# Kernel tuning notes

Measured on AMD Instinct MI355X. Metric: run time of the kernel, lower is better.

## Reference

```python
import jax, jax.numpy as jnp
import numpy as np

NUM_HEADS = 12
ROPE_BASE = 10000.0


def _rope_cache(u, v, head_dim):
    # u, v: [n, L] normalized coords; P pairs per axis = head_dim // 4
    P = head_dim // 2 // 2
    freqs = jnp.arange(P) / (P - 1 + 1e-09)
    inv = 1.0 / ROPE_BASE ** freqs
    ang_x = jnp.einsum('nl,f->nlf', u, inv)
    ang_y = jnp.einsum('nl,f->nlf', v, inv)
    return jnp.cos(ang_x), jnp.sin(ang_x), jnp.cos(ang_y), jnp.sin(ang_y)


def _rope_apply(t, cos_x, sin_x, cos_y, sin_y):
    # t: [n, L, H, D]
    n, L, H, D = t.shape
    q = t.reshape(n, L, H, D // 2, 2)
    ppa = (D // 2) // 2  # pairs per axis
    qx, qy = jnp.split(q, [ppa], axis=-2)

    def rotate(qp, c, s):
        c = c[:, :, None, :]
        s = s[:, :, None, :]
        x, y = qp[..., 0], qp[..., 1]
        return jnp.stack([x * c - y * s, x * s + y * c], axis=-1)

    qx = rotate(qx, cos_x, sin_x)
    qy = rotate(qy, cos_y, sin_y)
    return jnp.concatenate([qx, qy], axis=-2).reshape(n, L, H, D)


def setup_inputs() -> dict:
    key = jax.random.key(0)
    ks = jax.random.split(key, 10)
    n, L, d = 16, 1024, 768
    H = NUM_HEADS
    D = d // H
    glorot = jax.nn.initializers.xavier_uniform()
    return {
        'inputs_q': jax.random.normal(ks[0], (n, L, d), jnp.float32),
        'inputs_kv': jax.random.normal(ks[1], (n, L, d), jnp.float32),
        'Wq': glorot(ks[2], (d, H, D), jnp.float32),
        'bq': jnp.zeros((H, D), jnp.float32),
        'Wk': glorot(ks[3], (d, H, D), jnp.float32),
        'bk': jnp.zeros((H, D), jnp.float32),
        'Wv': glorot(ks[4], (d, H, D), jnp.float32),
        'bv': jnp.zeros((H, D), jnp.float32),
        'Wo': glorot(ks[5], (H, D, d), jnp.float32),
        'bo': jnp.zeros((d,), jnp.float32),
    }


def reference(inputs_q, inputs_kv, Wq, bq, Wk, bk, Wv, bv, Wo, bo):
    n, L, d = inputs_q.shape
    H = NUM_HEADS
    D = d // H

    q = jnp.einsum('nld,dhk->nlhk', inputs_q, Wq) + bq
    k = jnp.einsum('nld,dhk->nlhk', inputs_kv, Wk) + bk
    v = jnp.einsum('nld,dhk->nlhk', inputs_kv, Wv) + bv

    # square-grid 2D RoPE coordinates (rope_uv=None fallback)
    h = w = int(np.sqrt(L))
    ys, xs = np.mgrid[:h, :w]
    u = jnp.tile(((xs.reshape(-1) + 0.5) / w).astype(np.float32)[None, :], (n, 1))
    vv = jnp.tile(((ys.reshape(-1) + 0.5) / h).astype(np.float32)[None, :], (n, 1))
    cos_x, sin_x, cos_y, sin_y = _rope_cache(u, vv, D)

    q = _rope_apply(q, cos_x, sin_x, cos_y, sin_y)
    k = _rope_apply(k, cos_x, sin_x, cos_y, sin_y)

    scale = 1.0 / jnp.sqrt(jnp.float32(D))
    attn_logits = jnp.einsum('nqhd,nkhd->nhqk', q, k) * scale
    attn = jax.nn.softmax(attn_logits, axis=-1)
    out = jnp.einsum('nhqk,nkhd->nqhd', attn, v)
    return jnp.einsum('nqhd,hdm->nqm', out, Wo) + bo
```

## Files before the change

kernel.cpp:

```cpp
#include <hip/hip_runtime.h>
#include <cmath>

#define DMODEL 768
#define SEQ    1024
#define NH     12
#define HDIM   64
#define MTOT   16384

typedef unsigned short ushort_t;
typedef __attribute__((ext_vector_type(8))) short short8v;
typedef __attribute__((ext_vector_type(4))) float f32x4;
typedef __attribute__((ext_vector_type(16))) float f32x16;
typedef __attribute__((ext_vector_type(2))) int i32x2v;

union v8u { short8v v; unsigned u[4]; };

__device__ __forceinline__ ushort_t bf16rn(float x) {
  unsigned u = __float_as_uint(x);
  return (ushort_t)((u + 0x7FFFu + ((u >> 16) & 1u)) >> 16);
}
__device__ __forceinline__ void bsplit(float x, ushort_t& h, ushort_t& l) {
  h = bf16rn(x);
  float hf = __uint_as_float((unsigned)h << 16);
  l = bf16rn(x - hf);
}

__device__ __forceinline__ unsigned cvt_pk_bf16(float a, float b) {
  unsigned r;
  asm("v_cvt_pk_bf16_f32 %0, %1, %2" : "=v"(r) : "v"(a), "v"(b));
  return r;
}
__device__ __forceinline__ void bsplit2(float x0, float x1, unsigned& hw, unsigned& lw) {
  hw = cvt_pk_bf16(x0, x1);
  const float h0 = __uint_as_float(hw << 16);
  const float h1 = __uint_as_float(hw & 0xFFFF0000u);
  lw = cvt_pk_bf16(x0 - h0, x1 - h1);
}

__device__ __forceinline__ i32x2v pl32(unsigned a, unsigned b) {
  return __builtin_amdgcn_permlane32_swap((int)a, (int)b, false, false);
}

__device__ __forceinline__ void gld16(const void* g, void* l) {
  __builtin_amdgcn_global_load_lds(
      (const __attribute__((address_space(1))) int*)g,
      (__attribute__((address_space(3))) int*)l, 16, 0, 0);
}

__global__ __launch_bounds__(256)
void rope_table_kernel(float* __restrict__ tab) {
  int idx = blockIdx.x * 256 + threadIdx.x;
  if (idx >= SEQ * 16) return;
  int l = idx >> 4, p = idx & 15;
  double u = ((double)(l & 31) + 0.5) / 32.0;
  double v = ((double)(l >> 5) + 0.5) / 32.0;
  double freq = (double)p / (15.0 + 1e-9);
  double inv = pow(10000.0, -freq);
  tab[idx]         = (float)cos(u * inv);
  tab[16384 + idx] = (float)sin(u * inv);
  tab[32768 + idx] = (float)cos(v * inv);
  tab[49152 + idx] = (float)sin(v * inv);
}

__global__ __launch_bounds__(256)
void split_x_kernel(const float* __restrict__ X, ushort_t* __restrict__ H,
                    ushort_t* __restrict__ L) {
  const int i = blockIdx.x * 256 + threadIdx.x;
  const float4 a = ((const float4*)X)[i * 2];
  const float4 b = ((const float4*)X)[i * 2 + 1];
  v8u h, l;
  bsplit2(a.x, a.y, h.u[0], l.u[0]);
  bsplit2(a.z, a.w, h.u[1], l.u[1]);
  bsplit2(b.x, b.y, h.u[2], l.u[2]);
  bsplit2(b.z, b.w, h.u[3], l.u[3]);
  ((short8v*)H)[i] = h.v;
  ((short8v*)L)[i] = l.v;
}

__global__ __launch_bounds__(256)
void wsplit_t_kernel(const float* __restrict__ W, ushort_t* __restrict__ TH,
                     ushort_t* __restrict__ TL) {
  __shared__ __align__(16) float T[64][65];
  const int t = threadIdx.x;
  const int kt = blockIdx.x, nt = blockIdx.y;
  const int r = t >> 2, c4 = (t & 3) * 16;
  const float* src = W + (size_t)(kt * 64 + r) * DMODEL + nt * 64 + c4;
#pragma unroll
  for (int i = 0; i < 16; i += 4)
    *(float4*)&T[r][c4 + i] = *(const float4*)&src[i];
  __syncthreads();
  short8v h0, h1, l0, l1;
#pragma unroll
  for (int i = 0; i < 8; ++i) {
    ushort_t hh, ll;
    bsplit(T[c4 + i][r], hh, ll);
    h0[i] = (short)hh; l0[i] = (short)ll;
  }
#pragma unroll
  for (int i = 0; i < 8; ++i) {
    ushort_t hh, ll;
    bsplit(T[c4 + 8 + i][r], hh, ll);
    h1[i] = (short)hh; l1[i] = (short)ll;
  }
  const size_t o = (size_t)(nt * 64 + r) * DMODEL + kt * 64 + c4;
  *(short8v*)&TH[o] = h0; *(short8v*)&TH[o + 8] = h1;
  *(short8v*)&TL[o] = l0; *(short8v*)&TL[o + 8] = l1;
}

__global__ __launch_bounds__(256)
void gemm_mfma_kernel(const ushort_t* __restrict__ Ahi, const ushort_t* __restrict__ Alo,
                      const ushort_t* __restrict__ Bhi, const ushort_t* __restrict__ Blo,
                      const float* __restrict__ bias, float* __restrict__ Cout,
                      ushort_t* __restrict__ Ohi, ushort_t* __restrict__ Olo,
                      const float* __restrict__ rope, int mode, float oscale) {
  __shared__ __align__(16) ushort_t Ah[128][32];
  __shared__ __align__(16) ushort_t Al[128][32];
  __shared__ __align__(16) ushort_t Bh[128][32];
  __shared__ __align__(16) ushort_t Bl[128][32];

  const int t = threadIdx.x, lane = t & 63, w = t >> 6;
  const int l15 = lane & 15, l4 = lane >> 4;
  const int wm = w >> 1, wn = w & 1;
  const int m0 = blockIdx.x * 128, n0 = blockIdx.y * 128;

  const int crow = t >> 2, ccc = (t & 3) * 8;
  const ushort_t* pAh0 = Ahi + (size_t)(m0 + crow) * DMODEL + ccc;
  const ushort_t* pAh1 = pAh0 + (size_t)64 * DMODEL;
  const ushort_t* pAl0 = Alo + (size_t)(m0 + crow) * DMODEL + ccc;
  const ushort_t* pAl1 = pAl0 + (size_t)64 * DMODEL;
  const ushort_t* pBh0 = Bhi + (size_t)(n0 + crow) * DMODEL + ccc;
  const ushort_t* pBh1 = pBh0 + (size_t)64 * DMODEL;
  const ushort_t* pBl0 = Blo + (size_t)(n0 + crow) * DMODEL + ccc;
  const ushort_t* pBl1 = pBl0 + (size_t)64 * DMODEL;
  void* dAh0 = &Ah[crow][ccc];      void* dAh1 = &Ah[crow + 64][ccc];
  void* dAl0 = &Al[crow][ccc];      void* dAl1 = &Al[crow + 64][ccc];
  void* dBh0 = &Bh[crow][ccc];      void* dBh1 = &Bh[crow + 64][ccc];
  void* dBl0 = &Bl[crow][ccc];      void* dBl1 = &Bl[crow + 64][ccc];

  f32x4 acc[4][4] = {};

  for (int ks = 0; ks < DMODEL / 32; ++ks) {
    __syncthreads();
    gld16(pAh0, dAh0); gld16(pAh1, dAh1);
    gld16(pAl0, dAl0); gld16(pAl1, dAl1);
    gld16(pBh0, dBh0); gld16(pBh1, dBh1);
    gld16(pBl0, dBl0); gld16(pBl1, dBl1);
    pAh0 += 32; pAh1 += 32; pAl0 += 32; pAl1 += 32;
    pBh0 += 32; pBh1 += 32; pBl0 += 32; pBl1 += 32;
    __syncthreads();

    short8v afh[4], afl[4], bfh[4], bfl[4];
#pragma unroll
    for (int f = 0; f < 4; ++f) {
      afh[f] = *(const short8v*)&Ah[wm * 64 + f * 16 + l15][l4 * 8];
      afl[f] = *(const short8v*)&Al[wm * 64 + f * 16 + l15][l4 * 8];
      bfh[f] = *(const short8v*)&Bh[wn * 64 + f * 16 + l15][l4 * 8];
      bfl[f] = *(const short8v*)&Bl[wn * 64 + f * 16 + l15][l4 * 8];
    }
#pragma unroll
    for (int mf = 0; mf < 4; ++mf)
#pragma unroll
      for (int nf = 0; nf < 4; ++nf) {
        acc[mf][nf] = __builtin_amdgcn_mfma_f32_16x16x32_bf16(afh[mf], bfh[nf], acc[mf][nf], 0, 0, 0);
        acc[mf][nf] = __builtin_amdgcn_mfma_f32_16x16x32_bf16(afl[mf], bfh[nf], acc[mf][nf], 0, 0, 0);
        acc[mf][nf] = __builtin_amdgcn_mfma_f32_16x16x32_bf16(afh[mf], bfl[nf], acc[mf][nf], 0, 0, 0);
      }
  }

  float bcol[4];
#pragma unroll
  for (int nf = 0; nf < 4; ++nf) bcol[nf] = bias[n0 + wn * 64 + nf * 16 + l15];

  if (mode == 0) {
#pragma unroll
    for (int mf = 0; mf < 4; ++mf)
#pragma unroll
      for (int r = 0; r < 4; ++r) {
        const int m = m0 + wm * 64 + mf * 16 + l4 * 4 + r;
#pragma unroll
        for (int nf = 0; nf < 4; ++nf)
          Cout[(size_t)m * DMODEL + n0 + wn * 64 + nf * 16 + l15] = acc[mf][nf][r] + bcol[nf];
      }
  } else {
    const int h = blockIdx.y * 2 + wn;
#pragma unroll
    for (int mf = 0; mf < 4; ++mf)
#pragma unroll
      for (int r = 0; r < 4; ++r) {
        const int m = m0 + wm * 64 + mf * 16 + l4 * 4 + r;
        const int l = m & (SEQ - 1);
        const int nb = m >> 10;
        const size_t orow = ((size_t)(nb * NH + h) * SEQ + l) * HDIM;
        float vv[4];
#pragma unroll
        for (int nf = 0; nf < 4; ++nf) {
          float v = acc[mf][nf][r] + bcol[nf];
          if (mode == 1) {
            const float vp = __shfl_xor(v, 1, 64);
            const int tb = (nf < 2) ? 0 : 32768;
            const int pi = (nf & 1) * 8 + (l15 >> 1);
            const float c = rope[tb + l * 16 + pi];
            const float s = rope[tb + 16384 + l * 16 + pi];
            v = (l15 & 1) ? (vp * s + v * c) : (v * c - vp * s);
            v *= oscale;
          }
          vv[nf] = v;
        }
        unsigned h01, l01, h23, l23;
        bsplit2(vv[0], vv[1], h01, l01);
        bsplit2(vv[2], vv[3], h23, l23);
        Ohi[orow + 0 * 16 + l15] = (ushort_t)(h01 & 0xFFFFu);
        Ohi[orow + 1 * 16 + l15] = (ushort_t)(h01 >> 16);
        Ohi[orow + 2 * 16 + l15] = (ushort_t)(h23 & 0xFFFFu);
        Ohi[orow + 3 * 16 + l15] = (ushort_t)(h23 >> 16);
        Olo[orow + 0 * 16 + l15] = (ushort_t)(l01 & 0xFFFFu);
        Olo[orow + 1 * 16 + l15] = (ushort_t)(l01 >> 16);
        Olo[orow + 2 * 16 + l15] = (ushort_t)(l23 & 0xFFFFu);
        Olo[orow + 3 * 16 + l15] = (ushort_t)(l23 >> 16);
      }
  }
}

__global__ __launch_bounds__(256)
void vtrans_kernel(const ushort_t* __restrict__ VH, const ushort_t* __restrict__ VL,
                   ushort_t* __restrict__ TH, ushort_t* __restrict__ TL) {
  __shared__ __align__(16) ushort_t Th[64][72];
  __shared__ __align__(16) ushort_t Tl[64][72];
  const int t = threadIdx.x;
  const int lt = blockIdx.x, h = blockIdx.y, n = blockIdx.z;
  const int r = t >> 2, c = (t & 3) * 16;
  const size_t src = ((size_t)(n * NH + h) * SEQ + lt * 64 + r) * HDIM + c;
  *(short8v*)&Th[r][c]     = *(const short8v*)&VH[src];
  *(short8v*)&Th[r][c + 8] = *(const short8v*)&VH[src + 8];
  *(short8v*)&Tl[r][c]     = *(const short8v*)&VL[src];
  *(short8v*)&Tl[r][c + 8] = *(const short8v*)&VL[src + 8];
  __syncthreads();
  short8v h0, h1, l0, l1;
#pragma unroll
  for (int i = 0; i < 8; ++i) { h0[i] = (short)Th[c + i][r];     l0[i] = (short)Tl[c + i][r]; }
#pragma unroll
  for (int i = 0; i < 8; ++i) { h1[i] = (short)Th[c + 8 + i][r]; l1[i] = (short)Tl[c + 8 + i][r]; }
  const size_t dst = ((size_t)(n * NH + h) * HDIM + r) * SEQ + lt * 64 + c;
  *(short8v*)&TH[dst]     = h0; *(short8v*)&TH[dst + 8] = h1;
  *(short8v*)&TL[dst]     = l0; *(short8v*)&TL[dst + 8] = l1;
}

__global__ __launch_bounds__(256)
void attn_mfma_kernel(const ushort_t* __restrict__ qh, const ushort_t* __restrict__ ql,
                      const ushort_t* __restrict__ kh, const ushort_t* __restrict__ kl,
                      const ushort_t* __restrict__ vth, const ushort_t* __restrict__ vtl,
                      ushort_t* __restrict__ abh, ushort_t* __restrict__ abl) {
  __shared__ __align__(16) ushort_t KHs[2][64][64];
  __shared__ __align__(16) ushort_t KLs[2][64][64];
  __shared__ __align__(16) ushort_t VHs[2][64][64];
  __shared__ __align__(16) ushort_t VLs[2][64][64];

  const int t = threadIdx.x;
  const int lane = t & 63, w = t >> 6;
  const int l31 = lane & 31, l1 = lane >> 5;

  const int bid = blockIdx.x;
  const int xcd = bid & 7, rest = bid >> 3;
  const int qt = rest & 7;
  const int hl = (rest >> 3) * 8 + xcd;
  const int h = hl % NH, n = hl / NH;

  const size_t base = (size_t)(n * NH + h) * (SEQ * HDIM);

  short8v qfh[4], qfl[4];
  {
    const size_t qoff = base + (size_t)(qt * 128 + w * 32 + l31) * HDIM + l1 * 8;
#pragma unroll
    for (int ks = 0; ks < 4; ++ks) {
      qfh[ks] = *(const short8v*)&qh[qoff + ks * 16];
      qfl[ks] = *(const short8v*)&ql[qoff + ks * 16];
    }
  }

  const int srow = lane >> 3;
  const int schk = (lane & 7) ^ srow;
  const int sA = 2 * w, sB = 2 * w + 1;
  const size_t kofA = base + (size_t)(sA * 8 + srow) * HDIM + schk * 8;
  const size_t kofB = base + (size_t)(sB * 8 + srow) * HDIM + schk * 8;
  const size_t vofA = base + (size_t)(sA * 8 + srow) * SEQ + schk * 8;
  const size_t vofB = base + (size_t)(sB * 8 + srow) * SEQ + schk * 8;
  const int drA = sA * 8 + srow, drB = sB * 8 + srow, dc = (lane & 7) * 8;

  f32x16 Oa0 = {}, Oa1 = {};
  float mrun = -INFINITY, lp = 0.f;

#define ATTN_ISSUE(kt_, b_) do {                                            \
    const size_t ko_ = (size_t)(kt_) * (64 * HDIM);                         \
    const size_t vo_ = (size_t)(kt_) * 64;                                  \
    gld16(kh  + kofA + ko_, &KHs[b_][drA][dc]);                             \
    gld16(kh  + kofB + ko_, &KHs[b_][drB][dc]);                             \
    gld16(kl  + kofA + ko_, &KLs[b_][drA][dc]);                             \
    gld16(kl  + kofB + ko_, &KLs[b_][drB][dc]);                             \
    gld16(vth + vofA + vo_, &VHs[b_][drA][dc]);                             \
    gld16(vth + vofB + vo_, &VHs[b_][drB][dc]);                             \
    gld16(vtl + vofA + vo_, &VLs[b_][drA][dc]);                             \
    gld16(vtl + vofB + vo_, &VLs[b_][drB][dc]);                             \
  } while (0)

  ATTN_ISSUE(0, 0);

  for (int kt = 0; kt < 16; ++kt) {
    const int cur = kt & 1;
    __syncthreads();
    if (kt < 15) ATTN_ISSUE(kt + 1, cur ^ 1);

    f32x16 S0 = {}, S1 = {};
    __builtin_amdgcn_s_setprio(1);
#pragma unroll
    for (int ks = 0; ks < 4; ++ks) {
      const int cc = ((2 * ks + l1) ^ (l31 & 7)) * 8;
      const short8v k0h = *(const short8v*)&KHs[cur][l31][cc];
      const short8v k0l = *(const short8v*)&KLs[cur][l31][cc];
      const short8v k1h = *(const short8v*)&KHs[cur][32 + l31][cc];
      const short8v k1l = *(const short8v*)&KLs[cur][32 + l31][cc];
      S0 = __builtin_amdgcn_mfma_f32_32x32x16_bf16(k0h, qfh[ks], S0, 0, 0, 0);
      S1 = __builtin_amdgcn_mfma_f32_32x32x16_bf16(k1h, qfh[ks], S1, 0, 0, 0);
      S0 = __builtin_amdgcn_mfma_f32_32x32x16_bf16(k0l, qfh[ks], S0, 0, 0, 0);
      S1 = __builtin_amdgcn_mfma_f32_32x32x16_bf16(k1l, qfh[ks], S1, 0, 0, 0);
      S0 = __builtin_amdgcn_mfma_f32_32x32x16_bf16(k0h, qfl[ks], S0, 0, 0, 0);
      S1 = __builtin_amdgcn_mfma_f32_32x32x16_bf16(k1h, qfl[ks], S1, 0, 0, 0);
    }
    __builtin_amdgcn_s_setprio(0);

    float m01[16];
#pragma unroll
    for (int i = 0; i < 16; ++i) m01[i] = fmaxf(S0[i], S1[i]);
    float mx = fmaxf(fmaxf(fmaxf(m01[0], m01[1]), fmaxf(m01[2], m01[3])),
                     fmaxf(fmaxf(m01[4], m01[5]), fmaxf(m01[6], m01[7])));
    mx = fmaxf(mx, fmaxf(fmaxf(fmaxf(m01[8], m01[9]),  fmaxf(m01[10], m01[11])),
                         fmaxf(fmaxf(m01[12], m01[13]), fmaxf(m01[14], m01[15]))));
    if (__all(mx <= mrun + 11.5f)) {
#pragma unroll
      for (int i = 0; i < 16; ++i) {
        S0[i] = __builtin_amdgcn_exp2f(S0[i] - mrun);
        S1[i] = __builtin_amdgcn_exp2f(S1[i] - mrun);
      }
      f32x16 ts = S0 + S1;
      lp += ((((ts[0]+ts[1])+(ts[2]+ts[3]))+((ts[4]+ts[5])+(ts[6]+ts[7])))
           + (((ts[8]+ts[9])+(ts[10]+ts[11]))+((ts[12]+ts[13])+(ts[14]+ts[15]))));
    } else {
      const float om = fmaxf(mx, __shfl_xor(mx, 32));
      const float nm = fmaxf(mrun, om);
      const float scl = __builtin_amdgcn_exp2f(mrun - nm);
      mrun = nm;
#pragma unroll
      for (int i = 0; i < 16; ++i) {
        S0[i] = __builtin_amdgcn_exp2f(S0[i] - nm);
        S1[i] = __builtin_amdgcn_exp2f(S1[i] - nm);
      }
      f32x16 ts = S0 + S1;
      lp = lp * scl
         + ((((ts[0]+ts[1])+(ts[2]+ts[3]))+((ts[4]+ts[5])+(ts[6]+ts[7])))
          + (((ts[8]+ts[9])+(ts[10]+ts[11]))+((ts[12]+ts[13])+(ts[14]+ts[15]))));
      Oa0 = Oa0 * scl;
      Oa1 = Oa1 * scl;
    }

#pragma unroll
    for (int half = 0; half < 2; ++half) {
      unsigned hx[4], hy[4], lx[4], ly[4];
#pragma unroll
      for (int m = 0; m < 4; ++m) {
        float p0, p1, p2, p3;
        if (half == 0) { p0 = S0[4*m]; p1 = S0[4*m+1]; p2 = S0[4*m+2]; p3 = S0[4*m+3]; }
        else           { p0 = S1[4*m]; p1 = S1[4*m+1]; p2 = S1[4*m+2]; p3 = S1[4*m+3]; }
        bsplit2(p0, p1, hx[m], lx[m]);
        bsplit2(p2, p3, hy[m], ly[m]);
      }
      __builtin_amdgcn_s_setprio(1);
#pragma unroll
      for (int kss = 0; kss < 2; ++kss) {
        const i32x2v rhx = pl32(hx[2*kss], hx[2*kss+1]);
        const i32x2v rhy = pl32(hy[2*kss], hy[2*kss+1]);
        const i32x2v rlx = pl32(lx[2*kss], lx[2*kss+1]);
        const i32x2v rly = pl32(ly[2*kss], ly[2*kss+1]);
        v8u bfh, bfl;
        bfh.u[0] = (unsigned)rhx[0]; bfh.u[1] = (unsigned)rhy[0];
        bfh.u[2] = (unsigned)rhx[1]; bfh.u[3] = (unsigned)rhy[1];
        bfl.u[0] = (unsigned)rlx[0]; bfl.u[1] = (unsigned)rly[0];
        bfl.u[2] = (unsigned)rlx[1]; bfl.u[3] = (unsigned)rly[1];
        const int cc = ((4*half + 2*kss + l1) ^ (l31 & 7)) * 8;
        const short8v v0h = *(const short8v*)&VHs[cur][l31][cc];
        const short8v v0l = *(const short8v*)&VLs[cur][l31][cc];
        const short8v v1h = *(const short8v*)&VHs[cur][32 + l31][cc];
        const short8v v1l = *(const short8v*)&VLs[cur][32 + l31][cc];
        Oa0 = __builtin_amdgcn_mfma_f32_32x32x16_bf16(v0h, bfh.v, Oa0, 0, 0, 0);
        Oa1 = __builtin_amdgcn_mfma_f32_32x32x16_bf16(v1h, bfh.v, Oa1, 0, 0, 0);
        Oa0 = __builtin_amdgcn_mfma_f32_32x32x16_bf16(v0l, bfh.v, Oa0, 0, 0, 0);
        Oa1 = __builtin_amdgcn_mfma_f32_32x32x16_bf16(v1l, bfh.v, Oa1, 0, 0, 0);
        Oa0 = __builtin_amdgcn_mfma_f32_32x32x16_bf16(v0h, bfl.v, Oa0, 0, 0, 0);
        Oa1 = __builtin_amdgcn_mfma_f32_32x32x16_bf16(v1h, bfl.v, Oa1, 0, 0, 0);
      }
      __builtin_amdgcn_s_setprio(0);
    }
  }

  lp += __shfl_xor(lp, 32);
  const float inv = 1.0f / lp;
  const size_t orow = ((size_t)n * SEQ + qt * 128 + w * 32 + l31) * DMODEL + h * HDIM;
#pragma unroll
  for (int jd = 0; jd < 2; ++jd) {
#pragma unroll
    for (int g = 0; g < 4; ++g) {
      float o0, o1, o2, o3;
      if (jd == 0) { o0 = Oa0[4*g]; o1 = Oa0[4*g+1]; o2 = Oa0[4*g+2]; o3 = Oa0[4*g+3]; }
      else         { o0 = Oa1[4*g]; o1 = Oa1[4*g+1]; o2 = Oa1[4*g+2]; o3 = Oa1[4*g+3]; }
      o0 *= inv; o1 *= inv; o2 *= inv; o3 *= inv;
      unsigned h01, l01, h23, l23;
      bsplit2(o0, o1, h01, l01);
      bsplit2(o2, o3, h23, l23);
      const int d = 32 * jd + 8 * g + 4 * l1;
      uint2 sh; sh.x = h01; sh.y = h23;
      uint2 sl; sl.x = l01; sl.y = l23;
      *(uint2*)&abh[orow + d] = sh;
      *(uint2*)&abl[orow + d] = sl;
    }
  }
#undef ATTN_ISSUE
}

extern "C" void kernel_launch(void* const* d_in, const int* in_sizes, int n_in,
                              void* d_out, int out_size, void* d_ws, size_t ws_size,
                              hipStream_t stream) {
  (void)in_sizes; (void)n_in; (void)out_size;
  const float* Xq  = (const float*)d_in[0];
  const float* Xkv = (const float*)d_in[1];
  const float* Wq  = (const float*)d_in[2];
  const float* bq  = (const float*)d_in[3];
  const float* Wk  = (const float*)d_in[4];
  const float* bk  = (const float*)d_in[5];
  const float* Wv  = (const float*)d_in[6];
  const float* bv  = (const float*)d_in[7];
  const float* Wo  = (const float*)d_in[8];
  const float* bo  = (const float*)d_in[9];
  float* out = (float*)d_out;

  if (ws_size < 201588736ull) return;
  char* W = (char*)d_ws;
  const size_t HB = 25165824ull;
  float*    rope = (float*)W;
  ushort_t* xh  = (ushort_t*)(W + 262144);
  ushort_t* xl  = (ushort_t*)(W + 262144 + HB);
  ushort_t* vth = xh;
  ushort_t* vtl = xl;
  char* C0 = W + 262144 + 2 * HB;
  ushort_t* qhi = (ushort_t*)(C0);
  ushort_t* qlo = (ushort_t*)(C0 + HB);
  ushort_t* khi = (ushort_t*)(C0 + 2 * HB);
  ushort_t* klo = (ushort_t*)(C0 + 3 * HB);
  ushort_t* woth = (ushort_t*)(C0);
  ushort_t* wotl = woth + 589824;
  char* D0 = C0 + 4 * HB;
  ushort_t* vbh = (ushort_t*)(D0);
  ushort_t* vbl = (ushort_t*)(D0 + HB);
  ushort_t* abh = vbh;
  ushort_t* abl = vbl;
  ushort_t* wqth = (ushort_t*)d_out;            ushort_t* wqtl = wqth + 589824;
  ushort_t* wkth = wqth + 1179648;              ushort_t* wktl = wkth + 589824;
  ushort_t* wvth = wqth + 2359296;              ushort_t* wvtl = wvth + 589824;

  rope_table_kernel<<<64, 256, 0, stream>>>(rope);
  wsplit_t_kernel<<<dim3(12, 12), 256, 0, stream>>>(Wq, wqth, wqtl);
  wsplit_t_kernel<<<dim3(12, 12), 256, 0, stream>>>(Wk, wkth, wktl);
  wsplit_t_kernel<<<dim3(12, 12), 256, 0, stream>>>(Wv, wvth, wvtl);

  const dim3 gg(MTOT / 128, DMODEL / 128);
  const float q_scale = 0.125f * 1.44269504088896340736f;

  split_x_kernel<<<6144, 256, 0, stream>>>(Xq, xh, xl);
  gemm_mfma_kernel<<<gg, 256, 0, stream>>>(xh, xl, wqth, wqtl, bq, nullptr, qhi, qlo, rope, 1, q_scale);

  split_x_kernel<<<6144, 256, 0, stream>>>(Xkv, xh, xl);
  gemm_mfma_kernel<<<gg, 256, 0, stream>>>(xh, xl, wkth, wktl, bk, nullptr, khi, klo, rope, 1, 1.0f);
  gemm_mfma_kernel<<<gg, 256, 0, stream>>>(xh, xl, wvth, wvtl, bv, nullptr, vbh, vbl, rope, 2, 1.0f);

  vtrans_kernel<<<dim3(16, NH, 16), 256, 0, stream>>>(vbh, vbl, vth, vtl);

  attn_mfma_kernel<<<1536, 256, 0, stream>>>(qhi, qlo, khi, klo, vth, vtl, abh, abl);

  wsplit_t_kernel<<<dim3(12, 12), 256, 0, stream>>>(Wo, woth, wotl);
  gemm_mfma_kernel<<<gg, 256, 0, stream>>>(abh, abl, woth, wotl, bo, out, nullptr, nullptr, rope, 0, 1.0f);
}
```

Baseline: 573.7 us.

## Halve attention key tile to 32 and specialize loads per wave for occupancy

Result: slower. 677.6 us (+18.1%).

```diff
diff --git a/kernel.cpp b/kernel.cpp
--- a/kernel.cpp
+++ b/kernel.cpp
@@ -245,15 +245,15 @@
   *(short8v*)&TL[dst]     = l0; *(short8v*)&TL[dst + 8] = l1;
 }
 
-__global__ __launch_bounds__(256)
+__global__ __launch_bounds__(256, 4)
 void attn_mfma_kernel(const ushort_t* __restrict__ qh, const ushort_t* __restrict__ ql,
                       const ushort_t* __restrict__ kh, const ushort_t* __restrict__ kl,
                       const ushort_t* __restrict__ vth, const ushort_t* __restrict__ vtl,
                       ushort_t* __restrict__ abh, ushort_t* __restrict__ abl) {
-  __shared__ __align__(16) ushort_t KHs[2][64][64];
-  __shared__ __align__(16) ushort_t KLs[2][64][64];
-  __shared__ __align__(16) ushort_t VHs[2][64][64];
-  __shared__ __align__(16) ushort_t VLs[2][64][64];
+  __shared__ __align__(16) ushort_t KHs[2][32][64];
+  __shared__ __align__(16) ushort_t KLs[2][32][64];
+  __shared__ __align__(16) ushort_t VHs[2][64][32];
+  __shared__ __align__(16) ushort_t VLs[2][64][32];
 
   const int t = threadIdx.x;
   const int lane = t & 63, w = t >> 6;
@@ -277,100 +277,86 @@
     }
   }
 
-  const int srow = lane >> 3;
-  const int schk = (lane & 7) ^ srow;
-  const int sA = 2 * w, sB = 2 * w + 1;
-  const size_t kofA = base + (size_t)(sA * 8 + srow) * HDIM + schk * 8;
-  const size_t kofB = base + (size_t)(sB * 8 + srow) * HDIM + schk * 8;
-  const size_t vofA = base + (size_t)(sA * 8 + srow) * SEQ + schk * 8;
-  const size_t vofB = base + (size_t)(sB * 8 + srow) * SEQ + schk * 8;
-  const int drA = sA * 8 + srow, drB = sB * 8 + srow, dc = (lane & 7) * 8;
+  const int i = lane;
+  const int krow = i >> 3, kchk = (i & 7) ^ ((i >> 3) & 7);
+  const int vrow = i >> 2, vchk = (i & 3) ^ ((i >> 2) & 3);
 
   f32x16 Oa0 = {}, Oa1 = {};
   float mrun = -INFINITY, lp = 0.f;
 
-#define ATTN_ISSUE(kt_, b_) do {                                            \
-    const size_t ko_ = (size_t)(kt_) * (64 * HDIM);                         \
-    const size_t vo_ = (size_t)(kt_) * 64;                                  \
-    gld16(kh  + kofA + ko_, &KHs[b_][drA][dc]);                             \
-    gld16(kh  + kofB + ko_, &KHs[b_][drB][dc]);                             \
-    gld16(kl  + kofA + ko_, &KLs[b_][drA][dc]);                             \
-    gld16(kl  + kofB + ko_, &KLs[b_][drB][dc]);                             \
-    gld16(vth + vofA + vo_, &VHs[b_][drA][dc]);                             \
-    gld16(vth + vofB + vo_, &VHs[b_][drB][dc]);                             \
-    gld16(vtl + vofA + vo_, &VLs[b_][drA][dc]);                             \
-    gld16(vtl + vofB + vo_, &VLs[b_][drB][dc]);                             \
+#define ATTN_ISSUE(kt_, b_) do {                                               \
+    if (w == 0) {                                                              \
+      _Pragma("unroll")                                                        \
+      for (int j = 0; j < 4; ++j)                                              \
+        gld16(kh + base + (size_t)((kt_) * 32 + 8 * j + krow) * HDIM + kchk * 8, \
+              &KHs[b_][8 * j + krow][(i & 7) * 8]);                            \
+    } else if (w == 1) {                                                       \
+      _Pragma("unroll")                                                        \
+      for (int j = 0; j < 4; ++j)                                              \
+        gld16(kl + base + (size_t)((kt_) * 32 + 8 * j + krow) * HDIM + kchk * 8, \
+              &KLs[b_][8 * j + krow][(i & 7) * 8]);                            \
+    } else if (w == 2) {                                                       \
+      _Pragma("unroll")                                                        \
+      for (int j = 0; j < 4; ++j)                                              \
+        gld16(vth + base + (size_t)(16 * j + vrow) * SEQ + (kt_) * 32 + vchk * 8, \
+              &VHs[b_][16 * j + vrow][(i & 3) * 8]);                           \
+    } else {                                                                   \
+      _Pragma("unroll")                                                        \
+      for (int j = 0; j < 4; ++j)                                              \
+        gld16(vtl + base + (size_t)(16 * j + vrow) * SEQ + (kt_) * 32 + vchk * 8, \
+              &VLs[b_][16 * j + vrow][(i & 3) * 8]);                           \
+    }                                                                          \
   } while (0)
 
   ATTN_ISSUE(0, 0);
 
-  for (int kt = 0; kt < 16; ++kt) {
+  for (int kt = 0; kt < 32; ++kt) {
     const int cur = kt & 1;
     __syncthreads();
-    if (kt < 15) ATTN_ISSUE(kt + 1, cur ^ 1);
-
-    f32x16 S0 = {}, S1 = {};
+    if (kt < 31) ATTN_ISSUE(kt + 1, cur ^ 1);
+
+    f32x16 S0 = {};
     __builtin_amdgcn_s_setprio(1);
 #pragma unroll
     for (int ks = 0; ks < 4; ++ks) {
       const int cc = ((2 * ks + l1) ^ (l31 & 7)) * 8;
       const short8v k0h = *(const short8v*)&KHs[cur][l31][cc];
       const short8v k0l = *(const short8v*)&KLs[cur][l31][cc];
-      const short8v k1h = *(const short8v*)&KHs[cur][32 + l31][cc];
-      const short8v k1l = *(const short8v*)&KLs[cur][32 + l31][cc];
       S0 = __builtin_amdgcn_mfma_f32_32x32x16_bf16(k0h, qfh[ks], S0, 0, 0, 0);
-      S1 = __builtin_amdgcn_mfma_f32_32x32x16_bf16(k1h, qfh[ks], S1, 0, 0, 0);
       S0 = __builtin_amdgcn_mfma_f32_32x32x16_bf16(k0l, qfh[ks], S0, 0, 0, 0);
-      S1 = __builtin_amdgcn_mfma_f32_32x32x16_bf16(k1l, qfh[ks], S1, 0, 0, 0);
       S0 = __builtin_amdgcn_mfma_f32_32x32x16_bf16(k0h, qfl[ks], S0, 0, 0, 0);
-      S1 = __builtin_amdgcn_mfma_f32_32x32x16_bf16(k1h, qfl[ks], S1, 0, 0, 0);
     }
     __builtin_amdgcn_s_setprio(0);
 
-    float m01[16];
-#pragma unroll
-    for (int i = 0; i < 16; ++i) m01[i] = fmaxf(S0[i], S1[i]);
-    float mx = fmaxf(fmaxf(fmaxf(m01[0], m01[1]), fmaxf(m01[2], m01[3])),
-                     fmaxf(fmaxf(m01[4], m01[5]), fmaxf(m01[6], m01[7])));
-    mx = fmaxf(mx, fmaxf(fmaxf(fmaxf(m01[8], m01[9]),  fmaxf(m01[10], m01[11])),
-                         fmaxf(fmaxf(m01[12], m01[13]), fmaxf(m01[14], m01[15]))));
+    float mx = fmaxf(fmaxf(fmaxf(S0[0], S0[1]), fmaxf(S0[2], S0[3])),
+                     fmaxf(fmaxf(S0[4], S0[5]), fmaxf(S0[6], S0[7])));
+    mx = fmaxf(mx, fmaxf(fmaxf(fmaxf(S0[8], S0[9]),  fmaxf(S0[10], S0[11])),
+                         fmaxf(fmaxf(S0[12], S0[13]), fmaxf(S0[14], S0[15]))));
     if (__all(mx <= mrun + 11.5f)) {
 #pragma unroll
-      for (int i = 0; i < 16; ++i) {
-        S0[i] = __builtin_amdgcn_exp2f(S0[i] - mrun);
-        S1[i] = __builtin_amdgcn_exp2f(S1[i] - mrun);
-      }
-      f32x16 ts = S0 + S1;
-      lp += ((((ts[0]+ts[1])+(ts[2]+ts[3]))+((ts[4]+ts[5])+(ts[6]+ts[7])))
-           + (((ts[8]+ts[9])+(ts[10]+ts[11]))+((ts[12]+ts[13])+(ts[14]+ts[15]))));
+      for (int ii = 0; ii < 16; ++ii) S0[ii] = __builtin_amdgcn_exp2f(S0[ii] - mrun);
+      lp += ((((S0[0]+S0[1])+(S0[2]+S0[3]))+((S0[4]+S0[5])+(S0[6]+S0[7])))
+           + (((S0[8]+S0[9])+(S0[10]+S0[11]))+((S0[12]+S0[13])+(S0[14]+S0[15]))));
     } else {
       const float om = fmaxf(mx, __shfl_xor(mx, 32));
       const float nm = fmaxf(mrun, om);
       const float scl = __builtin_amdgcn_exp2f(mrun - nm);
       mrun = nm;
 #pragma unroll
-      for (int i = 0; i < 16; ++i) {
-        S0[i] = __builtin_amdgcn_exp2f(S0[i] - nm);
-        S1[i] = __builtin_amdgcn_exp2f(S1[i] - nm);
-      }
-      f32x16 ts = S0 + S1;
+      for (int ii = 0; ii < 16; ++ii) S0[ii] = __builtin_amdgcn_exp2f(S0[ii] - nm);
       lp = lp * scl
-         + ((((ts[0]+ts[1])+(ts[2]+ts[3]))+((ts[4]+ts[5])+(ts[6]+ts[7])))
-          + (((ts[8]+ts[9])+(ts[10]+ts[11]))+((ts[12]+ts[13])+(ts[14]+ts[15]))));
+         + ((((S0[0]+S0[1])+(S0[2]+S0[3]))+((S0[4]+S0[5])+(S0[6]+S0[7])))
+          + (((S0[8]+S0[9])+(S0[10]+S0[11]))+((S0[12]+S0[13])+(S0[14]+S0[15]))));
       Oa0 = Oa0 * scl;
       Oa1 = Oa1 * scl;
     }
 
-#pragma unroll
-    for (int half = 0; half < 2; ++half) {
+    {
       unsigned hx[4], hy[4], lx[4], ly[4];
 #pragma unroll
       for (int m = 0; m < 4; ++m) {
-        float p0, p1, p2, p3;
-        if (half == 0) { p0 = S0[4*m]; p1 = S0[4*m+1]; p2 = S0[4*m+2]; p3 = S0[4*m+3]; }
-        else           { p0 = S1[4*m]; p1 = S1[4*m+1]; p2 = S1[4*m+2]; p3 = S1[4*m+3]; }
-        bsplit2(p0, p1, hx[m], lx[m]);
-        bsplit2(p2, p3, hy[m], ly[m]);
+        bsplit2(S0[4*m],   S0[4*m+1], hx[m], lx[m]);
+        bsplit2(S0[4*m+2], S0[4*m+3], hy[m], ly[m]);
       }
       __builtin_amdgcn_s_setprio(1);
 #pragma unroll
@@ -384,7 +370,7 @@
         bfh.u[2] = (unsigned)rhx[1]; bfh.u[3] = (unsigned)rhy[1];
         bfl.u[0] = (unsigned)rlx[0]; bfl.u[1] = (unsigned)rly[0];
         bfl.u[2] = (unsigned)rlx[1]; bfl.u[3] = (unsigned)rly[1];
-        const int cc = ((4*half + 2*kss + l1) ^ (l31 & 7)) * 8;
+        const int cc = ((2*kss + l1) ^ (l31 & 3)) * 8;
         const short8v v0h = *(const short8v*)&VHs[cur][l31][cc];
         const short8v v0l = *(const short8v*)&VLs[cur][l31][cc];
         const short8v v1h = *(const short8v*)&VHs[cur][32 + l31][cc];
```
